# Optimization experiments

Measured on AMD Instinct MI355X. Metric: run time of the kernel, lower is better.

## Reference

```python
import jax, jax.numpy as jnp
import numpy as np

B, C, L = 32, 128, 4096
TIME_DIM = 512
K_TOP = 8


def setup_inputs() -> dict:
    key = jax.random.key(0)
    k1, k2, k3, k4 = jax.random.split(key, 4)
    x = jax.random.normal(k1, (B, C, L), dtype=jnp.float32)
    time_emb = jax.random.normal(k2, (B, TIME_DIM), dtype=jnp.float32)
    # nn.Linear(time_dim, channels): weight (C, time_dim), bias (C,)
    W = jax.random.normal(k3, (C, TIME_DIM), dtype=jnp.float32) / np.sqrt(TIME_DIM)
    b = jax.random.normal(k4, (C,), dtype=jnp.float32) * 0.01
    return {"x": x, "time_emb": time_emb, "W": W, "b": b}


def reference(x, time_emb, W, b):
    Bn, Cn, n = x.shape
    k = min(K_TOP, n // 2 + 1)
    # time-conditioned modulation: Linear -> tanh -> (1 + tanh) scale
    scale = time_emb @ W.T + b                      # (B, C)
    x_mod = x * (1.0 + jnp.tanh(scale))[:, :, None]  # (B, C, L)
    # rFFT along time
    x_fft = jnp.fft.rfft(x_mod, axis=-1)             # (B, C, F) complex64
    amp = jnp.abs(x_fft)
    # top-k frequency bins per (b, c) row
    _, topk_idx = jax.lax.top_k(amp, k)              # (B, C, k)
    gathered = jnp.take_along_axis(x_fft, topk_idx, axis=-1)
    bi = jnp.arange(Bn)[:, None, None]
    ci = jnp.arange(Cn)[None, :, None]
    masked_fft = jnp.zeros_like(x_fft).at[bi, ci, topk_idx].set(gathered)
    p_it = jnp.fft.irfft(masked_fft, n=n, axis=-1)
    return p_it.astype(x.dtype)
```

## Files before the change

### kernel.cpp

```cpp
#include <hip/hip_runtime.h>

#define LL 4096
#define THREADS 512
#define KK 8

typedef float v2f __attribute__((ext_vector_type(2)));

#define PD(i) ((i) + ((i) >> 4))
#define PERM8(r) ((((r) & 3) << 1) | ((r) >> 2))

__device__ __forceinline__ float sinr(float x) {
    float r; asm("v_sin_f32 %0, %1" : "=v"(r) : "v"(x)); return r;
}
__device__ __forceinline__ float cosr(float x) {
    float r; asm("v_cos_f32 %0, %1" : "=v"(r) : "v"(x)); return r;
}

__device__ __forceinline__ v2f padd(v2f a, v2f b) {
    v2f d; asm("v_pk_add_f32 %0, %1, %2" : "=v"(d) : "v"(a), "v"(b)); return d;
}
__device__ __forceinline__ v2f psub(v2f a, v2f b) {
    v2f d; asm("v_pk_add_f32 %0, %1, %2 neg_lo:[0,1] neg_hi:[0,1]" : "=v"(d) : "v"(a), "v"(b)); return d;
}
__device__ __forceinline__ v2f pmul(v2f a, v2f b) {
    v2f d; asm("v_pk_mul_f32 %0, %1, %2" : "=v"(d) : "v"(a), "v"(b)); return d;
}
__device__ __forceinline__ v2f addmi(v2f a, v2f b) {
    v2f d; asm("v_pk_add_f32 %0, %1, %2 op_sel:[0,1] op_sel_hi:[1,0] neg_hi:[0,1]" : "=v"(d) : "v"(a), "v"(b)); return d;
}
__device__ __forceinline__ v2f submi(v2f a, v2f b) {
    v2f d; asm("v_pk_add_f32 %0, %1, %2 op_sel:[0,1] op_sel_hi:[1,0] neg_lo:[0,1]" : "=v"(d) : "v"(a), "v"(b)); return d;
}
__device__ __forceinline__ v2f negi(v2f a) {
    v2f d; asm("v_pk_add_f32 %0, %1, 0 op_sel:[1,0] op_sel_hi:[0,0] neg_hi:[1,0]" : "=v"(d) : "v"(a)); return d;
}
__device__ __forceinline__ v2f pfma(v2f a, v2f b, v2f c) {
    v2f d; asm("v_pk_fma_f32 %0, %1, %2, %3" : "=v"(d) : "v"(a), "v"(b), "v"(c)); return d;
}
__device__ __forceinline__ v2f pfms(v2f a, v2f b, v2f c) {
    v2f d; asm("v_pk_fma_f32 %0, %1, %2, %3 neg_lo:[0,0,1] neg_hi:[0,0,1]" : "=v"(d) : "v"(a), "v"(b), "v"(c)); return d;
}
__device__ __forceinline__ v2f cmul(v2f a, v2f b) {
    v2f t, d;
    asm("v_pk_mul_f32 %0, %1, %2 op_sel:[0,0] op_sel_hi:[0,1]" : "=v"(t) : "v"(a), "v"(b));
    asm("v_pk_fma_f32 %0, %1, %2, %3 op_sel:[1,1,0] op_sel_hi:[1,0,1] neg_lo:[1,0,0]"
        : "=v"(d) : "v"(a), "v"(b), "v"(t));
    return d;
}
__device__ __forceinline__ v2f cmulw(v2f z, v2f w) {
    v2f t, d;
    asm("v_pk_mul_f32 %0, %1, %2 op_sel:[0,0] op_sel_hi:[1,0]" : "=v"(t) : "v"(z), "v"(w));
    asm("v_pk_fma_f32 %0, %1, %2, %3 op_sel:[1,1,0] op_sel_hi:[0,1,1] neg_hi:[1,0,0]"
        : "=v"(d) : "v"(z), "v"(w), "v"(t));
    return d;
}
__device__ __forceinline__ v2f unt0(v2f z, v2f y) {
    v2f d; asm("v_pk_add_f32 %0, %1, %2 neg_hi:[0,1]" : "=v"(d) : "v"(z), "v"(y)); return d;
}
__device__ __forceinline__ v2f unt1(v2f z, v2f y) {
    v2f d; asm("v_pk_add_f32 %0, %1, %2 op_sel:[1,1] op_sel_hi:[0,0] neg_hi:[1,0]" : "=v"(d) : "v"(z), "v"(y)); return d;
}

__device__ __forceinline__ void dft4(v2f& a, v2f& b, v2f& c, v2f& d) {
    v2f t0 = padd(a, c), t1 = psub(a, c);
    v2f t2 = padd(b, d), t3 = psub(b, d);
    a = padd(t0, t2); c = psub(t0, t2);
    b = addmi(t1, t3); d = submi(t1, t3);
}

__device__ __forceinline__ void dft8(v2f* v) {
    dft4(v[0], v[2], v[4], v[6]);
    dft4(v[1], v[3], v[5], v[7]);
    const float C2 = 0.70710678118654752f;
    const v2f W81 = (v2f){C2, C2};
    const v2f W83 = (v2f){-C2, C2};
    v[3] = cmulw(v[3], W81);
    v[5] = negi(v[5]);
    v[7] = cmulw(v[7], W83);
#pragma unroll
    for (int k0 = 0; k0 < 4; ++k0) {
        v2f a = v[2 * k0], b = v[2 * k0 + 1];
        v[2 * k0]     = padd(a, b);
        v[2 * k0 + 1] = psub(a, b);
    }
}

__device__ __forceinline__ void twiddle7(v2f* v, float th) {
    v2f w1 = (v2f){cosr(th), sinr(th)};
    v2f w2 = cmul(w1, w1);
    v2f w3 = cmul(w2, w1);
    v2f w4 = cmul(w2, w2);
    v2f w5 = cmul(w3, w2);
    v2f w6 = cmul(w3, w3);
    v2f w7 = cmul(w4, w3);
    v[1] = cmulw(v[1], w1);
    v[2] = cmulw(v[2], w2);
    v[3] = cmulw(v[3], w3);
    v[4] = cmulw(v[4], w4);
    v[5] = cmulw(v[5], w5);
    v[6] = cmulw(v[6], w6);
    v[7] = cmulw(v[7], w7);
}

#define DPP_STEP(CTRL)                                                          \
  {                                                                             \
    int vs_ = __builtin_amdgcn_update_dpp(__float_as_int(bv), __float_as_int(bv), \
                                          CTRL, 0xf, 0xf, false);               \
    int bs_ = __builtin_amdgcn_update_dpp(bb, bb, CTRL, 0xf, 0xf, false);       \
    float vf_ = __int_as_float(vs_);                                            \
    bool tk_ = (vf_ > bv) || (vf_ == bv && bs_ < bb);                           \
    bv = tk_ ? vf_ : bv; bb = tk_ ? bs_ : bb;                                   \
  }
#define DPP_ADD(CTRL)                                                           \
  ps += __int_as_float(__builtin_amdgcn_update_dpp(0, __float_as_int(ps),       \
                                                   CTRL, 0xf, 0xf, true));

__global__ __launch_bounds__(THREADS, 8)
void fft2_topk_k(const float* __restrict__ x, const float* __restrict__ te,
                 const float* __restrict__ W, const float* __restrict__ bias,
                 float* __restrict__ out) {
    __shared__ v2f zb[4353];
    __shared__ float wv[8];
    __shared__ float candV[2][16];
    __shared__ int   candB[2][16];
    __shared__ v2f  selAB[2][KK];
    __shared__ int  selF[2][KK];
    __shared__ v2f  T1[64], T2[64];

    int t = threadIdx.x;
    int pair = blockIdx.x;
    int b = pair >> 6;
    int c0 = (pair & 63) << 1;
    int row0 = (b << 7) + c0;

    {
        int mh = t >> 8, tt = t & 255;
        const float* tp = te + b * 512;
        const float* wp = W + (c0 + mh) * 512;
        float ps = tp[tt] * wp[tt] + tp[tt + 256] * wp[tt + 256];
        DPP_ADD(0x111) DPP_ADD(0x112) DPP_ADD(0x114) DPP_ADD(0x118)
        DPP_ADD(0x142) DPP_ADD(0x143)
        if ((t & 63) == 63) wv[t >> 6] = ps;
    }
    if (t < 64) {
        float a = (float)t * (1.0f / 64.0f);
        T1[t] = (v2f){cosr(a), sinr(a)};
    } else if (t < 128) {
        float a = (float)(t - 64) * (1.0f / 4096.0f);
        T2[t - 64] = (v2f){cosr(a), sinr(a)};
    }

    const float* xp0 = x + (size_t)row0 * LL;
    const float* xp1 = xp0 + LL;
    v2f v[8];
#pragma unroll
    for (int r = 0; r < 8; ++r) { v[r].x = xp0[t + 512 * r]; v[r].y = xp1[t + 512 * r]; }

    dft8(v);
    {
        int wb = 8 * t + (t >> 1);
#pragma unroll
        for (int r = 0; r < 8; ++r) zb[wb + r] = v[PERM8(r)];
    }
    __syncthreads();

    int rb = t + (t >> 4);

#pragma unroll
    for (int r = 0; r < 8; ++r) v[r] = zb[rb + 544 * r];
    twiddle7(v, (float)(t & 7) * (1.0f / 64.0f));
    dft8(v);
    __syncthreads();
    {
        int wb = 64 * (t >> 3) + (t & 7);
        int B0 = wb + (wb >> 4);
        int B1 = (wb + 8) + ((wb + 8) >> 4);
#pragma unroll
        for (int s = 0; s < 4; ++s) {
            zb[B0 + 17 * s] = v[PERM8(2 * s)];
            zb[B1 + 17 * s] = v[PERM8(2 * s + 1)];
        }
    }
    __syncthreads();

#pragma unroll
    for (int r = 0; r < 8; ++r) v[r] = zb[rb + 544 * r];
    twiddle7(v, (float)(t & 63) * (1.0f / 512.0f));
    dft8(v);
    __syncthreads();
    {
        int wb = 512 * (t >> 6) + (t & 63);
        int B2 = wb + (wb >> 4);
#pragma unroll
        for (int r = 0; r < 8; ++r) zb[B2 + 68 * r] = v[PERM8(r)];
    }
    __syncthreads();

#pragma unroll
    for (int r = 0; r < 8; ++r) v[r] = zb[rb + 544 * r];
    twiddle7(v, (float)t * (1.0f / 4096.0f));
    dft8(v);
#pragma unroll
    for (int r = 0; r < 8; ++r) zb[rb + 544 * r] = v[PERM8(r)];
    if (t == 0) zb[4352] = v[0];
    __syncthreads();

    int wid = t >> 6, lane = t & 63;

    if (wid < 4) {
        int row = wid >> 1, hf = wid & 1;
        int kb = (hf << 10) + lane;
        int base1 = PD(kb);
        int base2 = PD(4096 - kb);
        float amp[16];
        float lv = -1.f; int lm = 0;
#pragma unroll
        for (int m = 0; m < 16; ++m) {
            v2f z = zb[base1 + 68 * m];
            v2f y = zb[base2 - 68 * m];
            v2f X = row ? unt1(z, y) : unt0(z, y);
            float a = fmaf(X.x, X.x, X.y * X.y);
            amp[m] = a;
            if (a > lv) { lv = a; lm = m; }
        }
        for (int it = 0; it < KK; ++it) {
            float bv = lv; int bb = kb + (lm << 6);
            DPP_STEP(0x111)
            DPP_STEP(0x112)
            DPP_STEP(0x114)
            DPP_STEP(0x118)
            DPP_STEP(0x142)
            DPP_STEP(0x143)
            float vwin = __int_as_float(__builtin_amdgcn_readlane(__float_as_int(bv), 63));
            int   wbin = __builtin_amdgcn_readlane(bb, 63);
            if (lane == 0) { candV[row][(hf << 3) + it] = vwin; candB[row][(hf << 3) + it] = wbin; }
            if ((wbin & 63) == lane) {
                int m0 = ((wbin - (hf << 10)) >> 6);
                lv = -1.f; lm = 0;
#pragma unroll
                for (int m = 0; m < 16; ++m) {
                    float a = (m == m0) ? -1.f : amp[m];
                    amp[m] = a;
                    if (a > lv) { lv = a; lm = m; }
                }
            }
        }
    }
    __syncthreads();

    if (wid < 2 && lane < 17) {
        int row = wid;
        float g = 1.0f + tanhf(wv[4 * row] + wv[4 * row + 1] + wv[4 * row + 2]
                               + wv[4 * row + 3] + bias[c0 + row]);
        v2f z2 = zb[PD(2048)];
        float xn = 2.f * (row ? z2.y : z2.x);
        float a2048 = xn * xn;
        float myv; int myb, rank;
        if (lane < 16) {
            myv = candV[row][lane]; myb = candB[row][lane];
            rank = lane & 7;
            int ob = (lane < 8) ? 8 : 0;
#pragma unroll
            for (int j = 0; j < 8; ++j) {
                float ov = candV[row][ob + j]; int obn = candB[row][ob + j];
                if (ov > myv || (ov == myv && obn < myb)) rank++;
            }
            if (a2048 > myv) rank++;
        } else {
            myv = a2048; myb = 2048; rank = 0;
#pragma unroll
            for (int j = 0; j < 16; ++j)
                if (candV[row][j] >= myv) rank++;
        }
        if (rank < KK) {
            v2f z = zb[PD(myb)];
            v2f y = zb[PD(4096 - myb)];
            v2f X;
            if (row == 0) X = (v2f){0.5f * (z.x + y.x), 0.5f * (z.y - y.y)};
            else          X = (v2f){0.5f * (z.y + y.y), 0.5f * (y.x - z.x)};
            bool edge = (myb == 0) || (myb == 2048);
            float wgt = (edge ? 1.f : 2.f) * g * (1.0f / 4096.0f);
            selF[row][rank] = myb;
            selAB[row][rank] = (v2f){wgt * X.x, edge ? 0.f : wgt * X.y};
        }
    }
    __syncthreads();

    {
        int mh = t >> 8, u = t & 255;
        v2f rc[4], rp[4], tcv[4], sgv[4];
#pragma unroll
        for (int j = 0; j < 4; ++j) {
            int f0 = selF[mh][2 * j], f1 = selF[mh][2 * j + 1];
            v2f A0 = selAB[mh][2 * j], A1 = selAB[mh][2 * j + 1];
            int m0 = (f0 * u) & 4095, m1 = (f1 * u) & 4095;
            v2f e0 = cmul(T1[m0 >> 6], T2[m0 & 63]);
            v2f e1 = cmul(T1[m1 >> 6], T2[m1 & 63]);
            v2f w0 = cmul(A0, e0);
            v2f w1 = cmul(A1, e1);
            v2f s0 = T1[(f0 & 15) << 2];
            v2f s1 = T1[(f1 & 15) << 2];
            rc[j] = (v2f){w0.x, w1.x};
            rp[j] = (v2f){w0.x * s0.x + w0.y * s0.y, w1.x * s1.x + w1.y * s1.y};
            tcv[j] = (v2f){s0.x + s0.x, s1.x + s1.x};
            sgv[j] = (v2f){(f0 & 1) ? -1.f : 1.f, (f1 & 1) ? -1.f : 1.f};
        }
        float* op = out + (size_t)(row0 + mh) * LL;
#pragma unroll
        for (int q2 = 0; q2 < 8; ++q2) {
            v2f accv = padd(padd(rc[0], rc[1]), padd(rc[2], rc[3]));
            v2f acdv = pfma(rc[0], sgv[0],
                       pfma(rc[1], sgv[1],
                       pfma(rc[2], sgv[2], pmul(rc[3], sgv[3]))));
            op[u + (q2 << 8)] = accv.x + accv.y;
            op[u + (q2 << 8) + 2048] = acdv.x + acdv.y;
#pragma unroll
            for (int j = 0; j < 4; ++j) {
                v2f rn = pfms(tcv[j], rc[j], rp[j]);
                rp[j] = rc[j];
                rc[j] = rn;
            }
        }
    }
}

extern "C" void kernel_launch(void* const* d_in, const int* in_sizes, int n_in,
                              void* d_out, int out_size, void* d_ws, size_t ws_size,
                              hipStream_t stream) {
    const float* x    = (const float*)d_in[0];
    const float* te   = (const float*)d_in[1];
    const float* W    = (const float*)d_in[2];
    const float* bias = (const float*)d_in[3];
    float* out = (float*)d_out;
    fft2_topk_k<<<2048, THREADS, 0, stream>>>(x, te, W, bias, out);
}
```

Baseline: 46.77 us.

## Process two row pairs per block, overlapping second FFT with first inverse

Each block now handles four rows (two packed complex pairs) instead of two, halving the grid. The second pair's load and FFT passes are interleaved with the first pair's top-k merge and inverse synthesis, so the block never sits in a phase where only a few waves do work. Twiddle factors now come from the shared T1/T2 tables instead of per-pass sin/cos calls. The costs are higher register pressure from holding two pipelines' state at once and fewer blocks available to fill the GPU.

```diff
diff --git a/kernel.cpp b/kernel.cpp
--- a/kernel.cpp
+++ b/kernel.cpp
@@ -41,17 +41,17 @@
     v2f d; asm("v_pk_fma_f32 %0, %1, %2, %3 neg_lo:[0,0,1] neg_hi:[0,0,1]" : "=v"(d) : "v"(a), "v"(b), "v"(c)); return d;
 }
 __device__ __forceinline__ v2f cmul(v2f a, v2f b) {
-    v2f t, d;
-    asm("v_pk_mul_f32 %0, %1, %2 op_sel:[0,0] op_sel_hi:[0,1]" : "=v"(t) : "v"(a), "v"(b));
+    v2f t2, d;
+    asm("v_pk_mul_f32 %0, %1, %2 op_sel:[0,0] op_sel_hi:[0,1]" : "=v"(t2) : "v"(a), "v"(b));
     asm("v_pk_fma_f32 %0, %1, %2, %3 op_sel:[1,1,0] op_sel_hi:[1,0,1] neg_lo:[1,0,0]"
-        : "=v"(d) : "v"(a), "v"(b), "v"(t));
+        : "=v"(d) : "v"(a), "v"(b), "v"(t2));
     return d;
 }
 __device__ __forceinline__ v2f cmulw(v2f z, v2f w) {
-    v2f t, d;
-    asm("v_pk_mul_f32 %0, %1, %2 op_sel:[0,0] op_sel_hi:[1,0]" : "=v"(t) : "v"(z), "v"(w));
+    v2f t2, d;
+    asm("v_pk_mul_f32 %0, %1, %2 op_sel:[0,0] op_sel_hi:[1,0]" : "=v"(t2) : "v"(z), "v"(w));
     asm("v_pk_fma_f32 %0, %1, %2, %3 op_sel:[1,1,0] op_sel_hi:[0,1,1] neg_hi:[1,0,0]"
-        : "=v"(d) : "v"(z), "v"(w), "v"(t));
+        : "=v"(d) : "v"(z), "v"(w), "v"(t2));
     return d;
 }
 __device__ __forceinline__ v2f unt0(v2f z, v2f y) {
@@ -72,11 +72,9 @@
     dft4(v[0], v[2], v[4], v[6]);
     dft4(v[1], v[3], v[5], v[7]);
     const float C2 = 0.70710678118654752f;
-    const v2f W81 = (v2f){C2, C2};
-    const v2f W83 = (v2f){-C2, C2};
-    v[3] = cmulw(v[3], W81);
+    v[3] = cmulw(v[3], (v2f){C2, C2});
     v[5] = negi(v[5]);
-    v[7] = cmulw(v[7], W83);
+    v[7] = cmulw(v[7], (v2f){-C2, C2});
 #pragma unroll
     for (int k0 = 0; k0 < 4; ++k0) {
         v2f a = v[2 * k0], b = v[2 * k0 + 1];
@@ -85,8 +83,7 @@
     }
 }
 
-__device__ __forceinline__ void twiddle7(v2f* v, float th) {
-    v2f w1 = (v2f){cosr(th), sinr(th)};
+__device__ __forceinline__ void twiddle7w(v2f* v, v2f w1) {
     v2f w2 = cmul(w1, w1);
     v2f w3 = cmul(w2, w1);
     v2f w4 = cmul(w2, w2);
@@ -102,6 +99,46 @@
     v[7] = cmulw(v[7], w7);
 }
 
+__device__ __forceinline__ void inv_init(v2f* rc, v2f* rp, v2f* tcv, v2f* sgv,
+                                         const int* sF, const v2f* sAB,
+                                         const v2f* T1, const v2f* T2, int u) {
+#pragma unroll
+    for (int j = 0; j < 4; ++j) {
+        int f0 = sF[2 * j], f1 = sF[2 * j + 1];
+        v2f A0 = sAB[2 * j], A1 = sAB[2 * j + 1];
+        int m0 = (f0 * u) & 4095, m1 = (f1 * u) & 4095;
+        v2f e0 = cmul(T1[m0 >> 6], T2[m0 & 63]);
+        v2f e1 = cmul(T1[m1 >> 6], T2[m1 & 63]);
+        v2f w0 = cmul(A0, e0);
+        v2f w1 = cmul(A1, e1);
+        v2f s0 = T1[(f0 & 15) << 2];
+        v2f s1 = T1[(f1 & 15) << 2];
+        rc[j] = (v2f){w0.x, w1.x};
+        rp[j] = (v2f){w0.x * s0.x + w0.y * s0.y, w1.x * s1.x + w1.y * s1.y};
+        tcv[j] = (v2f){s0.x + s0.x, s1.x + s1.x};
+        sgv[j] = (v2f){(f0 & 1) ? -1.f : 1.f, (f1 & 1) ? -1.f : 1.f};
+    }
+}
+
+__device__ __forceinline__ void inv_run(v2f* rc, v2f* rp, const v2f* tcv,
+                                        const v2f* sgv, float* op, int u) {
+#pragma unroll
+    for (int q2 = 0; q2 < 8; ++q2) {
+        v2f accv = padd(padd(rc[0], rc[1]), padd(rc[2], rc[3]));
+        v2f acdv = pfma(rc[0], sgv[0],
+                   pfma(rc[1], sgv[1],
+                   pfma(rc[2], sgv[2], pmul(rc[3], sgv[3]))));
+        op[u + (q2 << 8)] = accv.x + accv.y;
+        op[u + (q2 << 8) + 2048] = acdv.x + acdv.y;
+#pragma unroll
+        for (int j = 0; j < 4; ++j) {
+            v2f rn = pfms(tcv[j], rc[j], rp[j]);
+            rp[j] = rc[j];
+            rc[j] = rn;
+        }
+    }
+}
+
 #define DPP_STEP(CTRL)                                                          \
   {                                                                             \
     int vs_ = __builtin_amdgcn_update_dpp(__float_as_int(bv), __float_as_int(bv), \
@@ -115,8 +152,117 @@
   ps += __int_as_float(__builtin_amdgcn_update_dpp(0, __float_as_int(ps),       \
                                                    CTRL, 0xf, 0xf, true));
 
+#define MOD_DOT(C0)                                                             \
+    {                                                                           \
+        int mh_ = t >> 8, tt_ = t & 255;                                        \
+        const float* tp_ = te + b * 512;                                        \
+        const float* wp_ = W + ((C0) + mh_) * 512;                              \
+        float ps = tp_[tt_] * wp_[tt_] + tp_[tt_ + 256] * wp_[tt_ + 256];       \
+        DPP_ADD(0x111) DPP_ADD(0x112) DPP_ADD(0x114) DPP_ADD(0x118)             \
+        DPP_ADD(0x142) DPP_ADD(0x143)                                           \
+        if ((t & 63) == 63) wv[t >> 6] = ps;                                    \
+    }
+
+#define GAIN(C0) ((wid < 2) ? 1.0f + tanhf(wv[4 * wid] + wv[4 * wid + 1]        \
+                   + wv[4 * wid + 2] + wv[4 * wid + 3] + bias[(C0) + wid]) : 0.f)
+
+#define PASS_READ(VV)                                                           \
+    _Pragma("unroll") for (int r = 0; r < 8; ++r) VV[r] = zb[rb + 544 * r];
+#define PASS0_WRITE(VV)                                                         \
+    { int wb_ = 8 * t + (t >> 1);                                               \
+      _Pragma("unroll") for (int r = 0; r < 8; ++r) zb[wb_ + r] = VV[PERM8(r)]; }
+#define PASS1_WRITE(VV)                                                         \
+    { int wb_ = 64 * (t >> 3) + (t & 7);                                        \
+      int B0_ = wb_ + (wb_ >> 4);                                               \
+      int B1_ = (wb_ + 8) + ((wb_ + 8) >> 4);                                   \
+      _Pragma("unroll") for (int s = 0; s < 4; ++s) {                           \
+          zb[B0_ + 17 * s] = VV[PERM8(2 * s)];                                  \
+          zb[B1_ + 17 * s] = VV[PERM8(2 * s + 1)]; } }
+#define PASS2_WRITE(VV)                                                         \
+    { int wb_ = 512 * (t >> 6) + (t & 63);                                      \
+      int B2_ = wb_ + (wb_ >> 4);                                               \
+      _Pragma("unroll") for (int r = 0; r < 8; ++r) zb[B2_ + 68 * r] = VV[PERM8(r)]; }
+#define PASS3_INPLACE(VV)                                                       \
+    { v2f w1_ = cmul(T1[t >> 6], T2[t & 63]);                                   \
+      PASS_READ(VV)                                                             \
+      twiddle7w(VV, w1_);                                                       \
+      dft8(VV);                                                                 \
+      _Pragma("unroll") for (int r = 0; r < 8; ++r) zb[rb + 544 * r] = VV[PERM8(r)]; \
+      if (t == 0) zb[4352] = VV[0]; }
+
+#define TOPK()                                                                  \
+    if (wid < 4) {                                                              \
+        int row_ = wid >> 1, hf_ = wid & 1;                                     \
+        int kb_ = (hf_ << 10) + lane;                                           \
+        int b1_ = PD(kb_), b2_ = PD(4096 - kb_);                                \
+        float amp_[16]; float lv_ = -1.f; int lm_ = 0;                          \
+        _Pragma("unroll")                                                       \
+        for (int m = 0; m < 16; ++m) {                                          \
+            v2f z_ = zb[b1_ + 68 * m], y_ = zb[b2_ - 68 * m];                   \
+            v2f X_ = row_ ? unt1(z_, y_) : unt0(z_, y_);                        \
+            float a_ = fmaf(X_.x, X_.x, X_.y * X_.y);                           \
+            amp_[m] = a_;                                                       \
+            if (a_ > lv_) { lv_ = a_; lm_ = m; }                                \
+        }                                                                       \
+        for (int it = 0; it < KK; ++it) {                                       \
+            float bv = lv_; int bb = kb_ + (lm_ << 6);                          \
+            DPP_STEP(0x111) DPP_STEP(0x112) DPP_STEP(0x114)                     \
+            DPP_STEP(0x118) DPP_STEP(0x142) DPP_STEP(0x143)                     \
+            float vw_ = __int_as_float(__builtin_amdgcn_readlane(__float_as_int(bv), 63)); \
+            int   wn_ = __builtin_amdgcn_readlane(bb, 63);                      \
+            if (lane == 0) { candV[row_][(hf_ << 3) + it] = vw_;                \
+                             candB[row_][(hf_ << 3) + it] = wn_; }              \
+            if ((wn_ & 63) == lane) {                                           \
+                int m0_ = ((wn_ - (hf_ << 10)) >> 6);                           \
+                lv_ = -1.f; lm_ = 0;                                            \
+                _Pragma("unroll")                                               \
+                for (int m = 0; m < 16; ++m) {                                  \
+                    float a_ = (m == m0_) ? -1.f : amp_[m];                     \
+                    amp_[m] = a_;                                               \
+                    if (a_ > lv_) { lv_ = a_; lm_ = m; }                        \
+                }                                                               \
+            }                                                                   \
+        }                                                                       \
+    }
+
+#define MERGE(G)                                                                \
+    if (wid < 2 && lane < 17) {                                                 \
+        int row_ = wid;                                                         \
+        v2f z2_ = zb[PD(2048)];                                                 \
+        float xn_ = 2.f * (row_ ? z2_.y : z2_.x);                               \
+        float a2_ = xn_ * xn_;                                                  \
+        float myv_; int myb_, rk_;                                              \
+        if (lane < 16) {                                                        \
+            myv_ = candV[row_][lane]; myb_ = candB[row_][lane];                 \
+            rk_ = lane & 7;                                                     \
+            int ob_ = (lane < 8) ? 8 : 0;                                       \
+            _Pragma("unroll")                                                   \
+            for (int j = 0; j < 8; ++j) {                                       \
+                float ov_ = candV[row_][ob_ + j]; int on_ = candB[row_][ob_ + j]; \
+                if (ov_ > myv_ || (ov_ == myv_ && on_ < myb_)) rk_++;           \
+            }                                                                   \
+            if (a2_ > myv_) rk_++;                                              \
+        } else {                                                                \
+            myv_ = a2_; myb_ = 2048; rk_ = 0;                                   \
+            _Pragma("unroll")                                                   \
+            for (int j = 0; j < 16; ++j)                                        \
+                if (candV[row_][j] >= myv_) rk_++;                              \
+        }                                                                       \
+        if (rk_ < KK) {                                                         \
+            v2f z_ = zb[PD(myb_)];                                              \
+            v2f y_ = zb[PD(4096 - myb_)];                                       \
+            v2f X_;                                                             \
+            if (row_ == 0) X_ = (v2f){0.5f * (z_.x + y_.x), 0.5f * (z_.y - y_.y)}; \
+            else           X_ = (v2f){0.5f * (z_.y + y_.y), 0.5f * (y_.x - z_.x)}; \
+            bool ed_ = (myb_ == 0) || (myb_ == 2048);                           \
+            float wg_ = (ed_ ? 1.f : 2.f) * (G) * (1.0f / 4096.0f);             \
+            selF[row_][rk_] = myb_;                                             \
+            selAB[row_][rk_] = (v2f){wg_ * X_.x, ed_ ? 0.f : wg_ * X_.y};       \
+        }                                                                       \
+    }
+
 __global__ __launch_bounds__(THREADS, 8)
-void fft2_topk_k(const float* __restrict__ x, const float* __restrict__ te,
+void fft4_topk_k(const float* __restrict__ x, const float* __restrict__ te,
                  const float* __restrict__ W, const float* __restrict__ bias,
                  float* __restrict__ out) {
     __shared__ v2f zb[4353];
@@ -128,20 +274,23 @@
     __shared__ v2f  T1[64], T2[64];
 
     int t = threadIdx.x;
-    int pair = blockIdx.x;
-    int b = pair >> 6;
-    int c0 = (pair & 63) << 1;
-    int row0 = (b << 7) + c0;
-
-    {
-        int mh = t >> 8, tt = t & 255;
-        const float* tp = te + b * 512;
-        const float* wp = W + (c0 + mh) * 512;
-        float ps = tp[tt] * wp[tt] + tp[tt + 256] * wp[tt + 256];
-        DPP_ADD(0x111) DPP_ADD(0x112) DPP_ADD(0x114) DPP_ADD(0x118)
-        DPP_ADD(0x142) DPP_ADD(0x143)
-        if ((t & 63) == 63) wv[t >> 6] = ps;
-    }
+    int wid = t >> 6, lane = t & 63;
+    int mh = t >> 8, u = t & 255;
+    int rb = t + (t >> 4);
+
+    int pA = blockIdx.x << 1;
+    int b = pA >> 6;
+    int c0A = (pA & 63) << 1;
+    int c0B = c0A + 2;
+    int row0A = (b << 7) + c0A;
+    int row0B = row0A + 2;
+
+    const float* xA0 = x + (size_t)row0A * LL;
+    const float* xA1 = xA0 + LL;
+    v2f v[8];
+#pragma unroll
+    for (int r = 0; r < 8; ++r) { v[r].x = xA0[t + 512 * r]; v[r].y = xA1[t + 512 * r]; }
+    MOD_DOT(c0A)
     if (t < 64) {
         float a = (float)t * (1.0f / 64.0f);
         T1[t] = (v2f){cosr(a), sinr(a)};
@@ -150,178 +299,59 @@
         T2[t - 64] = (v2f){cosr(a), sinr(a)};
     }
 
-    const float* xp0 = x + (size_t)row0 * LL;
-    const float* xp1 = xp0 + LL;
-    v2f v[8];
-#pragma unroll
-    for (int r = 0; r < 8; ++r) { v[r].x = xp0[t + 512 * r]; v[r].y = xp1[t + 512 * r]; }
-
     dft8(v);
-    {
-        int wb = 8 * t + (t >> 1);
-#pragma unroll
-        for (int r = 0; r < 8; ++r) zb[wb + r] = v[PERM8(r)];
-    }
-    __syncthreads();
-
-    int rb = t + (t >> 4);
-
-#pragma unroll
-    for (int r = 0; r < 8; ++r) v[r] = zb[rb + 544 * r];
-    twiddle7(v, (float)(t & 7) * (1.0f / 64.0f));
-    dft8(v);
-    __syncthreads();
-    {
-        int wb = 64 * (t >> 3) + (t & 7);
-        int B0 = wb + (wb >> 4);
-        int B1 = (wb + 8) + ((wb + 8) >> 4);
-#pragma unroll
-        for (int s = 0; s < 4; ++s) {
-            zb[B0 + 17 * s] = v[PERM8(2 * s)];
-            zb[B1 + 17 * s] = v[PERM8(2 * s + 1)];
-        }
-    }
-    __syncthreads();
-
-#pragma unroll
-    for (int r = 0; r < 8; ++r) v[r] = zb[rb + 544 * r];
-    twiddle7(v, (float)(t & 63) * (1.0f / 512.0f));
-    dft8(v);
-    __syncthreads();
-    {
-        int wb = 512 * (t >> 6) + (t & 63);
-        int B2 = wb + (wb >> 4);
-#pragma unroll
-        for (int r = 0; r < 8; ++r) zb[B2 + 68 * r] = v[PERM8(r)];
-    }
-    __syncthreads();
-
-#pragma unroll
-    for (int r = 0; r < 8; ++r) v[r] = zb[rb + 544 * r];
-    twiddle7(v, (float)t * (1.0f / 4096.0f));
-    dft8(v);
-#pragma unroll
-    for (int r = 0; r < 8; ++r) zb[rb + 544 * r] = v[PERM8(r)];
-    if (t == 0) zb[4352] = v[0];
-    __syncthreads();
-
-    int wid = t >> 6, lane = t & 63;
-
-    if (wid < 4) {
-        int row = wid >> 1, hf = wid & 1;
-        int kb = (hf << 10) + lane;
-        int base1 = PD(kb);
-        int base2 = PD(4096 - kb);
-        float amp[16];
-        float lv = -1.f; int lm = 0;
-#pragma unroll
-        for (int m = 0; m < 16; ++m) {
-            v2f z = zb[base1 + 68 * m];
-            v2f y = zb[base2 - 68 * m];
-            v2f X = row ? unt1(z, y) : unt0(z, y);
-            float a = fmaf(X.x, X.x, X.y * X.y);
-            amp[m] = a;
-            if (a > lv) { lv = a; lm = m; }
-        }
-        for (int it = 0; it < KK; ++it) {
-            float bv = lv; int bb = kb + (lm << 6);
-            DPP_STEP(0x111)
-            DPP_STEP(0x112)
-            DPP_STEP(0x114)
-            DPP_STEP(0x118)
-            DPP_STEP(0x142)
-            DPP_STEP(0x143)
-            float vwin = __int_as_float(__builtin_amdgcn_readlane(__float_as_int(bv), 63));
-            int   wbin = __builtin_amdgcn_readlane(bb, 63);
-            if (lane == 0) { candV[row][(hf << 3) + it] = vwin; candB[row][(hf << 3) + it] = wbin; }
-            if ((wbin & 63) == lane) {
-                int m0 = ((wbin - (hf << 10)) >> 6);
-                lv = -1.f; lm = 0;
-#pragma unroll
-                for (int m = 0; m < 16; ++m) {
-                    float a = (m == m0) ? -1.f : amp[m];
-                    amp[m] = a;
-                    if (a > lv) { lv = a; lm = m; }
-                }
-            }
-        }
-    }
-    __syncthreads();
-
-    if (wid < 2 && lane < 17) {
-        int row = wid;
-        float g = 1.0f + tanhf(wv[4 * row] + wv[4 * row + 1] + wv[4 * row + 2]
-                               + wv[4 * row + 3] + bias[c0 + row]);
-        v2f z2 = zb[PD(2048)];
-        float xn = 2.f * (row ? z2.y : z2.x);
-        float a2048 = xn * xn;
-        float myv; int myb, rank;
-        if (lane < 16) {
-            myv = candV[row][lane]; myb = candB[row][lane];
-            rank = lane & 7;
-            int ob = (lane < 8) ? 8 : 0;
-#pragma unroll
-            for (int j = 0; j < 8; ++j) {
-                float ov = candV[row][ob + j]; int obn = candB[row][ob + j];
-                if (ov > myv || (ov == myv && obn < myb)) rank++;
-            }
-            if (a2048 > myv) rank++;
-        } else {
-            myv = a2048; myb = 2048; rank = 0;
-#pragma unroll
-            for (int j = 0; j < 16; ++j)
-                if (candV[row][j] >= myv) rank++;
-        }
-        if (rank < KK) {
-            v2f z = zb[PD(myb)];
-            v2f y = zb[PD(4096 - myb)];
-            v2f X;
-            if (row == 0) X = (v2f){0.5f * (z.x + y.x), 0.5f * (z.y - y.y)};
-            else          X = (v2f){0.5f * (z.y + y.y), 0.5f * (y.x - z.x)};
-            bool edge = (myb == 0) || (myb == 2048);
-            float wgt = (edge ? 1.f : 2.f) * g * (1.0f / 4096.0f);
-            selF[row][rank] = myb;
-            selAB[row][rank] = (v2f){wgt * X.x, edge ? 0.f : wgt * X.y};
-        }
-    }
-    __syncthreads();
-
-    {
-        int mh = t >> 8, u = t & 255;
-        v2f rc[4], rp[4], tcv[4], sgv[4];
-#pragma unroll
-        for (int j = 0; j < 4; ++j) {
-            int f0 = selF[mh][2 * j], f1 = selF[mh][2 * j + 1];
-            v2f A0 = selAB[mh][2 * j], A1 = selAB[mh][2 * j + 1];
-            int m0 = (f0 * u) & 4095, m1 = (f1 * u) & 4095;
-            v2f e0 = cmul(T1[m0 >> 6], T2[m0 & 63]);
-            v2f e1 = cmul(T1[m1 >> 6], T2[m1 & 63]);
-            v2f w0 = cmul(A0, e0);
-            v2f w1 = cmul(A1, e1);
-            v2f s0 = T1[(f0 & 15) << 2];
-            v2f s1 = T1[(f1 & 15) << 2];
-            rc[j] = (v2f){w0.x, w1.x};
-            rp[j] = (v2f){w0.x * s0.x + w0.y * s0.y, w1.x * s1.x + w1.y * s1.y};
-            tcv[j] = (v2f){s0.x + s0.x, s1.x + s1.x};
-            sgv[j] = (v2f){(f0 & 1) ? -1.f : 1.f, (f1 & 1) ? -1.f : 1.f};
-        }
-        float* op = out + (size_t)(row0 + mh) * LL;
-#pragma unroll
-        for (int q2 = 0; q2 < 8; ++q2) {
-            v2f accv = padd(padd(rc[0], rc[1]), padd(rc[2], rc[3]));
-            v2f acdv = pfma(rc[0], sgv[0],
-                       pfma(rc[1], sgv[1],
-                       pfma(rc[2], sgv[2], pmul(rc[3], sgv[3]))));
-            op[u + (q2 << 8)] = accv.x + accv.y;
-            op[u + (q2 << 8) + 2048] = acdv.x + acdv.y;
-#pragma unroll
-            for (int j = 0; j < 4; ++j) {
-                v2f rn = pfms(tcv[j], rc[j], rp[j]);
-                rp[j] = rc[j];
-                rc[j] = rn;
-            }
-        }
-    }
+    PASS0_WRITE(v)
+    __syncthreads();
+    float g = GAIN(c0A);
+    { PASS_READ(v) twiddle7w(v, T1[t & 7]); dft8(v); }
+    __syncthreads();
+    PASS1_WRITE(v)
+    __syncthreads();
+    { PASS_READ(v) twiddle7w(v, cmul(T1[(t & 63) >> 3], T2[(t & 7) << 3])); dft8(v); }
+    __syncthreads();
+    PASS2_WRITE(v)
+    __syncthreads();
+    PASS3_INPLACE(v)
+    __syncthreads();
+
+    TOPK()
+    __syncthreads();
+
+    const float* xB0 = x + (size_t)row0B * LL;
+    const float* xB1 = xB0 + LL;
+    v2f vB[8];
+#pragma unroll
+    for (int r = 0; r < 8; ++r) { vB[r].x = xB0[t + 512 * r]; vB[r].y = xB1[t + 512 * r]; }
+    MERGE(g)
+    MOD_DOT(c0B)
+    __syncthreads();
+
+    dft8(vB);
+    PASS0_WRITE(vB)
+    __syncthreads();
+    g = GAIN(c0B);
+    { PASS_READ(vB) twiddle7w(vB, T1[t & 7]); dft8(vB); }
+    v2f rcA[4], rpA[4], tcA[4], sgA[4];
+    inv_init(rcA, rpA, tcA, sgA, &selF[mh][0], &selAB[mh][0], T1, T2, u);
+    __syncthreads();
+    PASS1_WRITE(vB)
+    __syncthreads();
+    { PASS_READ(vB) twiddle7w(vB, cmul(T1[(t & 63) >> 3], T2[(t & 7) << 3])); dft8(vB); }
+    inv_run(rcA, rpA, tcA, sgA, out + (size_t)(row0A + mh) * LL, u);
+    __syncthreads();
+    PASS2_WRITE(vB)
+    __syncthreads();
+    PASS3_INPLACE(vB)
+    __syncthreads();
+
+    TOPK()
+    __syncthreads();
+    MERGE(g)
+    __syncthreads();
+
+    v2f rcB[4], rpB[4], tcB[4], sgB[4];
+    inv_init(rcB, rpB, tcB, sgB, &selF[mh][0], &selAB[mh][0], T1, T2, u);
+    inv_run(rcB, rpB, tcB, sgB, out + (size_t)(row0B + mh) * LL, u);
 }
 
 extern "C" void kernel_launch(void* const* d_in, const int* in_sizes, int n_in,
@@ -332,5 +362,5 @@
     const float* W    = (const float*)d_in[2];
     const float* bias = (const float*)d_in[3];
     float* out = (float*)d_out;
-    fft2_topk_k<<<2048, THREADS, 0, stream>>>(x, te, W, bias, out);
-}
+    fft4_topk_k<<<1024, THREADS, 0, stream>>>(x, te, W, bias, out);
+}
```

Result: slower. 52.51 us (+12.3%).
